# Kernel optimization log

Measured on AMD Instinct MI355X. Metric: run time of the kernel, lower is better.

## Reference

```python
import jax, jax.numpy as jnp
import numpy as np

E = 384      # n_embed
H = 6        # n_head
HS = E // H  # head_size = 64
B = 64
T = 256      # == block_size
FF = 4 * E


def _layernorm(x, g, b, eps=1e-5):
    m = x.mean(-1, keepdims=True)
    v = ((x - m) ** 2).mean(-1, keepdims=True)
    return (x - m) / jnp.sqrt(v + eps) * g + b


def _mha(q_in, k_in, v_in, wq, bq, wk, bk, wv, bv, pw, pb):
    # Faithful to source: scale uses q_in's last dim (n_embed=384), NOT head_size,
    # and the causal tril mask is applied even in cross-attention.
    scale = q_in.shape[-1] ** -0.5
    q = jnp.einsum('bte,hes->bhts', q_in, wq) + bq[None, :, None, :]  # [B,H,T1,HS]
    k = jnp.einsum('bue,hes->bhus', k_in, wk) + bk[None, :, None, :]  # [B,H,T2,HS]
    v = jnp.einsum('bue,hes->bhus', v_in, wv) + bv[None, :, None, :]
    wei = jnp.einsum('bhts,bhus->bhtu', q, k) * scale                 # [B,H,T1,T2]
    T1, T2 = q_in.shape[1], k_in.shape[1]
    mask = jnp.tril(jnp.ones((T1, T2), dtype=bool))
    wei = jnp.where(mask[None, None], wei, -jnp.inf)
    wei = jax.nn.softmax(wei, axis=-1)
    out = jnp.einsum('bhtu,bhus->bths', wei, v)                       # [B,T1,H,HS]
    out = out.reshape(out.shape[0], out.shape[1], -1)                 # concat heads
    return out @ pw + pb


def setup_inputs() -> dict:
    key = jax.random.key(0)
    ks = jax.random.split(key, 32)
    s = 0.02
    d = {
        'encode_output': jax.random.normal(ks[0], (B, T, E), jnp.float32),
        'x': jax.random.normal(ks[1], (B, T, E), jnp.float32),
    }
    i = 2
    for p in ('sa1', 'sa2'):
        d[p + '_wq'] = jax.random.normal(ks[i], (H, E, HS), jnp.float32) * s; i += 1
        d[p + '_bq'] = jnp.zeros((H, HS), jnp.float32)
        d[p + '_wk'] = jax.random.normal(ks[i], (H, E, HS), jnp.float32) * s; i += 1
        d[p + '_bk'] = jnp.zeros((H, HS), jnp.float32)
        d[p + '_wv'] = jax.random.normal(ks[i], (H, E, HS), jnp.float32) * s; i += 1
        d[p + '_bv'] = jnp.zeros((H, HS), jnp.float32)
        d[p + '_pw'] = jax.random.normal(ks[i], (E, E), jnp.float32) * s; i += 1
        d[p + '_pb'] = jnp.zeros((E,), jnp.float32)
    d['ff_w1'] = jax.random.normal(ks[i], (E, FF), jnp.float32) * s; i += 1
    d['ff_b1'] = jnp.zeros((FF,), jnp.float32)
    d['ff_w2'] = jax.random.normal(ks[i], (FF, E), jnp.float32) * s; i += 1
    d['ff_b2'] = jnp.zeros((E,), jnp.float32)
    for n in ('ln1', 'ln2', 'ln3'):
        d[n + '_g'] = jnp.ones((E,), jnp.float32)
        d[n + '_b'] = jnp.zeros((E,), jnp.float32)
    return d


def reference(encode_output, x,
              sa1_wq, sa1_bq, sa1_wk, sa1_bk, sa1_wv, sa1_bv, sa1_pw, sa1_pb,
              sa2_wq, sa2_bq, sa2_wk, sa2_bk, sa2_wv, sa2_bv, sa2_pw, sa2_pb,
              ff_w1, ff_b1, ff_w2, ff_b2,
              ln1_g, ln1_b, ln2_g, ln2_b, ln3_g, ln3_b):
    # masked self-attention + add&norm
    a1 = _mha(x, x, x, sa1_wq, sa1_bq, sa1_wk, sa1_bk, sa1_wv, sa1_bv, sa1_pw, sa1_pb)
    o1 = _layernorm(x + a1, ln1_g, ln1_b)
    # cross-attention (q=o1, k=v=encode_output) + add&norm
    a2 = _mha(o1, encode_output, encode_output,
              sa2_wq, sa2_bq, sa2_wk, sa2_bk, sa2_wv, sa2_bv, sa2_pw, sa2_pb)
    o2 = _layernorm(o1 + a2, ln2_g, ln2_b)
    # FFN + add&norm
    f = jax.nn.relu(o2 @ ff_w1 + ff_b1) @ ff_w2 + ff_b2
    return _layernorm(o2 + f, ln3_g, ln3_b)
```

## Files before the change

### kernel.cpp

```cpp
#include <hip/hip_runtime.h>

typedef __attribute__((ext_vector_type(8))) short bf16x8;
typedef __attribute__((ext_vector_type(4))) float f32x4;

__device__ __forceinline__ float b2f(ushort b) {
    union { unsigned int u; float f; } x;
    x.u = ((unsigned int)b) << 16;
    return x.f;
}
__device__ __forceinline__ ushort f2b(float f) {
    union { float f; unsigned int u; } x;
    x.f = f;
    unsigned int r = x.u + 0x7fffu + ((x.u >> 16) & 1u);
    return (ushort)(r >> 16);
}
__device__ __forceinline__ int4 pack8(float4 a, float4 b) {
    union { int4 v; ushort u[8]; } r;
    r.u[0] = f2b(a.x); r.u[1] = f2b(a.y); r.u[2] = f2b(a.z); r.u[3] = f2b(a.w);
    r.u[4] = f2b(b.x); r.u[5] = f2b(b.y); r.u[6] = f2b(b.z); r.u[7] = f2b(b.w);
    return r.v;
}

__global__ __launch_bounds__(256) void gemm_bt(
    const ushort* __restrict__ A, const ushort* __restrict__ Bt,
    ushort* __restrict__ C, const float* __restrict__ bias,
    const ushort* __restrict__ resb, const float* __restrict__ resf,
    int M, int N, int K, int relu)
{
    __shared__ __align__(16) ushort As[128 * 32];
    __shared__ __align__(16) ushort Bs[128 * 32];
    const int tid  = threadIdx.x;
    const int wave = tid >> 6, lane = tid & 63;
    const int wm = wave >> 1, wn = wave & 1;
    const int qd = lane >> 4, lc = lane & 15;
    const int row0 = blockIdx.y * 128, col0 = blockIdx.x * 128;

    const int srow = tid >> 1;
    const int scol = (tid & 1) * 16;
    const ushort* Ag = A  + (size_t)(row0 + srow) * K + scol;
    const ushort* Bg = Bt + (size_t)(col0 + srow) * K + scol;
    ushort* Asd = &As[srow * 32 + scol];
    ushort* Bsd = &Bs[srow * 32 + scol];

    f32x4 acc[4][4];
#pragma unroll
    for (int i = 0; i < 4; i++)
#pragma unroll
        for (int j = 0; j < 4; j++) acc[i][j] = 0.0f;

    int4 a0 = *(const int4*)(Ag);
    int4 a1 = *(const int4*)(Ag + 8);
    int4 b0 = *(const int4*)(Bg);
    int4 b1 = *(const int4*)(Bg + 8);

    for (int k0 = 0; k0 < K; k0 += 32) {
        __syncthreads();
        *(int4*)Asd = a0; *(int4*)(Asd + 8) = a1;
        *(int4*)Bsd = b0; *(int4*)(Bsd + 8) = b1;
        if (k0 + 32 < K) {
            a0 = *(const int4*)(Ag + k0 + 32);
            a1 = *(const int4*)(Ag + k0 + 40);
            b0 = *(const int4*)(Bg + k0 + 32);
            b1 = *(const int4*)(Bg + k0 + 40);
        }
        __syncthreads();

        bf16x8 af[4], bfr[4];
#pragma unroll
        for (int mi = 0; mi < 4; mi++)
            af[mi] = *(const bf16x8*)&As[(wm * 64 + mi * 16 + lc) * 32 + qd * 8];
#pragma unroll
        for (int ni = 0; ni < 4; ni++)
            bfr[ni] = *(const bf16x8*)&Bs[(wn * 64 + ni * 16 + lc) * 32 + qd * 8];
#pragma unroll
        for (int mi = 0; mi < 4; mi++)
#pragma unroll
            for (int ni = 0; ni < 4; ni++)
                acc[mi][ni] = __builtin_amdgcn_mfma_f32_16x16x32_bf16(
                    af[mi], bfr[ni], acc[mi][ni], 0, 0, 0);
    }

#pragma unroll
    for (int mi = 0; mi < 4; mi++) {
#pragma unroll
        for (int r = 0; r < 4; r++) {
            int grow = row0 + wm * 64 + mi * 16 + qd * 4 + r;
#pragma unroll
            for (int ni = 0; ni < 4; ni++) {
                int gcol = col0 + wn * 64 + ni * 16 + lc;
                float v = acc[mi][ni][r];
                if (bias) v += bias[gcol];
                if (resb) v += b2f(resb[(size_t)grow * N + gcol]);
                if (resf) v += resf[(size_t)grow * N + gcol];
                if (relu) v = fmaxf(v, 0.0f);
                C[(size_t)grow * N + gcol] = f2b(v);
            }
        }
    }
}

__global__ __launch_bounds__(256) void gemm_n64(
    const ushort* __restrict__ A, const ushort* __restrict__ Bt,
    ushort* __restrict__ C, const float* __restrict__ bias,
    const ushort* __restrict__ resb, const float* __restrict__ resf,
    int M, int N, int K, int relu)
{
    __shared__ __align__(16) ushort As[128 * 32];
    __shared__ __align__(16) ushort Bs[64 * 32];
    const int tid  = threadIdx.x;
    const int wave = tid >> 6, lane = tid & 63;
    const int qd = lane >> 4, lc = lane & 15;
    const int row0 = blockIdx.y * 128, col0 = blockIdx.x * 64;

    const int srow = tid >> 1;
    const int scol = (tid & 1) * 16;
    const ushort* Ag = A + (size_t)(row0 + srow) * K + scol;
    ushort* Asd = &As[srow * 32 + scol];
    const int brow = tid >> 2;
    const int bcol = (tid & 3) * 8;
    const ushort* Bg = Bt + (size_t)(col0 + brow) * K + bcol;
    ushort* Bsd = &Bs[brow * 32 + bcol];

    f32x4 acc[2][4];
#pragma unroll
    for (int i = 0; i < 2; i++)
#pragma unroll
        for (int j = 0; j < 4; j++) acc[i][j] = 0.0f;

    int4 a0 = *(const int4*)(Ag);
    int4 a1 = *(const int4*)(Ag + 8);
    int4 b0 = *(const int4*)(Bg);

    for (int k0 = 0; k0 < K; k0 += 32) {
        __syncthreads();
        *(int4*)Asd = a0; *(int4*)(Asd + 8) = a1;
        *(int4*)Bsd = b0;
        if (k0 + 32 < K) {
            a0 = *(const int4*)(Ag + k0 + 32);
            a1 = *(const int4*)(Ag + k0 + 40);
            b0 = *(const int4*)(Bg + k0 + 32);
        }
        __syncthreads();

        bf16x8 af[2], bfr[4];
#pragma unroll
        for (int mi = 0; mi < 2; mi++)
            af[mi] = *(const bf16x8*)&As[(wave * 32 + mi * 16 + lc) * 32 + qd * 8];
#pragma unroll
        for (int ni = 0; ni < 4; ni++)
            bfr[ni] = *(const bf16x8*)&Bs[(ni * 16 + lc) * 32 + qd * 8];
#pragma unroll
        for (int mi = 0; mi < 2; mi++)
#pragma unroll
            for (int ni = 0; ni < 4; ni++)
                acc[mi][ni] = __builtin_amdgcn_mfma_f32_16x16x32_bf16(
                    af[mi], bfr[ni], acc[mi][ni], 0, 0, 0);
    }

#pragma unroll
    for (int mi = 0; mi < 2; mi++) {
#pragma unroll
        for (int r = 0; r < 4; r++) {
            int grow = row0 + wave * 32 + mi * 16 + qd * 4 + r;
#pragma unroll
            for (int ni = 0; ni < 4; ni++) {
                int gcol = col0 + ni * 16 + lc;
                float v = acc[mi][ni][r];
                if (bias) v += bias[gcol];
                if (resb) v += b2f(resb[(size_t)grow * N + gcol]);
                if (resf) v += resf[(size_t)grow * N + gcol];
                if (relu) v = fmaxf(v, 0.0f);
                C[(size_t)grow * N + gcol] = f2b(v);
            }
        }
    }
}

__global__ __launch_bounds__(256) void gemm_dual(
    const ushort* __restrict__ A1, const ushort* __restrict__ B1t,
    ushort* __restrict__ C1, const float* __restrict__ bias1, int N1,
    const ushort* __restrict__ A2, const ushort* __restrict__ B2t,
    ushort* __restrict__ C2, const float* __restrict__ bias2, int N2,
    int split, int K)
{
    __shared__ __align__(16) ushort As[128 * 32];
    __shared__ __align__(16) ushort Bs[64 * 32];
    const int tid  = threadIdx.x;
    const int wave = tid >> 6, lane = tid & 63;
    const int qd = lane >> 4, lc = lane & 15;
    const bool first = (int)blockIdx.x < split;
    const ushort* A  = first ? A1 : A2;
    const ushort* Bt = first ? B1t : B2t;
    ushort* C        = first ? C1 : C2;
    const float* bias = first ? bias1 : bias2;
    const int N      = first ? N1 : N2;
    const int col0   = (first ? blockIdx.x : blockIdx.x - split) * 64;
    const int row0   = blockIdx.y * 128;

    const int srow = tid >> 1;
    const int scol = (tid & 1) * 16;
    const ushort* Ag = A + (size_t)(row0 + srow) * K + scol;
    ushort* Asd = &As[srow * 32 + scol];
    const int brow = tid >> 2;
    const int bcol = (tid & 3) * 8;
    const ushort* Bg = Bt + (size_t)(col0 + brow) * K + bcol;
    ushort* Bsd = &Bs[brow * 32 + bcol];

    f32x4 acc[2][4];
#pragma unroll
    for (int i = 0; i < 2; i++)
#pragma unroll
        for (int j = 0; j < 4; j++) acc[i][j] = 0.0f;

    int4 a0 = *(const int4*)(Ag);
    int4 a1 = *(const int4*)(Ag + 8);
    int4 b0 = *(const int4*)(Bg);

    for (int k0 = 0; k0 < K; k0 += 32) {
        __syncthreads();
        *(int4*)Asd = a0; *(int4*)(Asd + 8) = a1;
        *(int4*)Bsd = b0;
        if (k0 + 32 < K) {
            a0 = *(const int4*)(Ag + k0 + 32);
            a1 = *(const int4*)(Ag + k0 + 40);
            b0 = *(const int4*)(Bg + k0 + 32);
        }
        __syncthreads();

        bf16x8 af[2], bfr[4];
#pragma unroll
        for (int mi = 0; mi < 2; mi++)
            af[mi] = *(const bf16x8*)&As[(wave * 32 + mi * 16 + lc) * 32 + qd * 8];
#pragma unroll
        for (int ni = 0; ni < 4; ni++)
            bfr[ni] = *(const bf16x8*)&Bs[(ni * 16 + lc) * 32 + qd * 8];
#pragma unroll
        for (int mi = 0; mi < 2; mi++)
#pragma unroll
            for (int ni = 0; ni < 4; ni++)
                acc[mi][ni] = __builtin_amdgcn_mfma_f32_16x16x32_bf16(
                    af[mi], bfr[ni], acc[mi][ni], 0, 0, 0);
    }

#pragma unroll
    for (int mi = 0; mi < 2; mi++) {
#pragma unroll
        for (int r = 0; r < 4; r++) {
            int grow = row0 + wave * 32 + mi * 16 + qd * 4 + r;
#pragma unroll
            for (int ni = 0; ni < 4; ni++) {
                int gcol = col0 + ni * 16 + lc;
                float v = acc[mi][ni][r] + bias[gcol];
                C[(size_t)grow * N + gcol] = f2b(v);
            }
        }
    }
}

__global__ __launch_bounds__(256) void attn(
    const ushort* __restrict__ q, int qstr,
    const ushort* __restrict__ k, int kstr,
    const ushort* __restrict__ v, int vstr,
    ushort* __restrict__ out)
{
    __shared__ __align__(16) ushort Qs[64 * 72];
    __shared__ __align__(16) ushort Kc[64 * 72];
    __shared__ __align__(16) ushort Vc[64 * 72];
    __shared__ __align__(16) ushort Ps[64 * 264];

    const int tid = threadIdx.x;
    const int wave = tid >> 6, lane = tid & 63;
    const int qd = lane >> 4, lc = lane & 15;
    const int b = blockIdx.z, h = blockIdx.y, t0 = blockIdx.x * 64;
    const int hc = h * 64;
    const float scale = 0.051031036307982884f;

    {
        int r = tid >> 2, c = (tid & 3) * 16;
        int4 q0 = *(const int4*)&q[(size_t)(b * 256 + t0 + r) * qstr + hc + c];
        int4 q1 = *(const int4*)&q[(size_t)(b * 256 + t0 + r) * qstr + hc + c + 8];
        *(int4*)&Qs[r * 72 + c] = q0;
        *(int4*)&Qs[r * 72 + c + 8] = q1;
    }

    f32x4 accS[16];
#pragma unroll
    for (int j = 0; j < 16; j++) accS[j] = 0.0f;

    for (int uc = 0; uc < 4; uc++) {
        int r = tid >> 2, c = (tid & 3) * 16;
        int4 k0v = *(const int4*)&k[(size_t)(b * 256 + uc * 64 + r) * kstr + hc + c];
        int4 k1v = *(const int4*)&k[(size_t)(b * 256 + uc * 64 + r) * kstr + hc + c + 8];
        __syncthreads();
        *(int4*)&Kc[r * 72 + c] = k0v;
        *(int4*)&Kc[r * 72 + c + 8] = k1v;
        __syncthreads();
#pragma unroll
        for (int s0 = 0; s0 < 64; s0 += 32) {
            bf16x8 a = *(const bf16x8*)&Qs[(wave * 16 + lc) * 72 + s0 + qd * 8];
#pragma unroll
            for (int ni = 0; ni < 4; ni++) {
                bf16x8 bb = *(const bf16x8*)&Kc[(ni * 16 + lc) * 72 + s0 + qd * 8];
                accS[uc * 4 + ni] =
                    __builtin_amdgcn_mfma_f32_16x16x32_bf16(a, bb, accS[uc * 4 + ni], 0, 0, 0);
            }
        }
    }

#pragma unroll
    for (int rr = 0; rr < 4; rr++) {
        int t = t0 + wave * 16 + qd * 4 + rr;
        float pv[16];
        float mx = -3.0e38f;
#pragma unroll
        for (int j = 0; j < 16; j++) {
            int u = (j >> 2) * 64 + (j & 3) * 16 + lc;
            float s = accS[j][rr] * scale;
            s = (u <= t) ? s : -3.0e38f;
            pv[j] = s;
            mx = fmaxf(mx, s);
        }
#pragma unroll
        for (int m = 1; m < 16; m <<= 1) mx = fmaxf(mx, __shfl_xor(mx, m, 16));
        float sum = 0.0f;
#pragma unroll
        for (int j = 0; j < 16; j++) { float p = __expf(pv[j] - mx); pv[j] = p; sum += p; }
#pragma unroll
        for (int m = 1; m < 16; m <<= 1) sum += __shfl_xor(sum, m, 16);
        float inv = 1.0f / sum;
#pragma unroll
        for (int j = 0; j < 16; j++) {
            int u = (j >> 2) * 64 + (j & 3) * 16 + lc;
            Ps[(wave * 16 + qd * 4 + rr) * 264 + u] = f2b(pv[j] * inv);
        }
    }

    f32x4 accO[4];
#pragma unroll
    for (int j = 0; j < 4; j++) accO[j] = 0.0f;
    for (int uc = 0; uc < 4; uc++) {
        int r = tid >> 2, s0 = (tid & 3) * 16;
        int4 v0 = *(const int4*)&v[(size_t)(b * 256 + uc * 64 + r) * vstr + hc + s0];
        int4 v1 = *(const int4*)&v[(size_t)(b * 256 + uc * 64 + r) * vstr + hc + s0 + 8];
        __syncthreads();
        {
            const ushort* t0p = (const ushort*)&v0;
            const ushort* t1p = (const ushort*)&v1;
#pragma unroll
            for (int j = 0; j < 8; j++) Vc[(s0 + j) * 72 + r] = t0p[j];
#pragma unroll
            for (int j = 0; j < 8; j++) Vc[(s0 + 8 + j) * 72 + r] = t1p[j];
        }
        __syncthreads();
#pragma unroll
        for (int u0 = 0; u0 < 64; u0 += 32) {
            bf16x8 a = *(const bf16x8*)&Ps[(wave * 16 + lc) * 264 + uc * 64 + u0 + qd * 8];
#pragma unroll
            for (int ni = 0; ni < 4; ni++) {
                bf16x8 bb = *(const bf16x8*)&Vc[(ni * 16 + lc) * 72 + u0 + qd * 8];
                accO[ni] = __builtin_amdgcn_mfma_f32_16x16x32_bf16(a, bb, accO[ni], 0, 0, 0);
            }
        }
    }

#pragma unroll
    for (int ni = 0; ni < 4; ni++)
#pragma unroll
        for (int rr = 0; rr < 4; rr++) {
            int t = t0 + wave * 16 + qd * 4 + rr;
            out[(size_t)(b * 256 + t) * 384 + hc + ni * 16 + lc] = f2b(accO[ni][rr]);
        }
}

__global__ __launch_bounds__(256) void lnorm(
    const ushort* __restrict__ in, const float* __restrict__ g,
    const float* __restrict__ be, ushort* __restrict__ outb,
    float* __restrict__ outf)
{
    const int wave = threadIdx.x >> 6, lane = threadIdx.x & 63;
    const int row = blockIdx.x * 4 + wave;
    const ushort* r = in + (size_t)row * 384;
    float x[6], s1 = 0.0f, s2 = 0.0f;
#pragma unroll
    for (int j = 0; j < 6; j++) {
        x[j] = b2f(r[j * 64 + lane]);
        s1 += x[j]; s2 += x[j] * x[j];
    }
#pragma unroll
    for (int m = 1; m < 64; m <<= 1) {
        s1 += __shfl_xor(s1, m, 64);
        s2 += __shfl_xor(s2, m, 64);
    }
    float mean = s1 * (1.0f / 384.0f);
    float var  = s2 * (1.0f / 384.0f) - mean * mean;
    float rstd = rsqrtf(var + 1e-5f);
#pragma unroll
    for (int j = 0; j < 6; j++) {
        float y = (x[j] - mean) * rstd * g[j * 64 + lane] + be[j * 64 + lane];
        if (outb) outb[(size_t)row * 384 + j * 64 + lane] = f2b(y);
        if (outf) outf[(size_t)row * 384 + j * 64 + lane] = y;
    }
}

__device__ __forceinline__ void dev_cvt(const float* in, ushort* out, int blk) {
    size_t i = ((size_t)blk * 256 + threadIdx.x) * 8;
    float4 a = *(const float4*)(in + i);
    float4 b = *(const float4*)(in + i + 4);
    *(int4*)(out + i) = pack8(a, b);
}
__device__ __forceinline__ void dev_transp(const float* in, ushort* out,
                                           int R, int C, int bx, int by,
                                           float (*t)[33]) {
    const int tx = threadIdx.x & 31, ty = threadIdx.x >> 5;
    const int c0 = bx * 32, r0 = by * 32;
#pragma unroll
    for (int i = 0; i < 32; i += 8)
        t[ty + i][tx] = in[(size_t)(r0 + ty + i) * C + c0 + tx];
    __syncthreads();
#pragma unroll
    for (int i = 0; i < 32; i += 8)
        out[(size_t)(c0 + ty + i) * R + r0 + tx] = f2b(t[tx][ty + i]);
}
__device__ __forceinline__ void dev_packqkv(const float* wq, const float* wk,
                                            const float* wv, ushort* Wt,
                                            int blk, float (*t)[33]) {
    const int tx = threadIdx.x & 31, ty = threadIdx.x >> 5;
    const int bx = blk % 12, by = (blk / 12) % 2, bz = blk / 24;
    const int e0 = bx * 32, s0 = by * 32;
    const int seg = bz / 6, h = bz - seg * 6;
    const float* w = (seg == 0) ? wq : (seg == 1) ? wk : wv;
    const float* wh = w + (size_t)h * 384 * 64;
#pragma unroll
    for (int i = 0; i < 32; i += 8)
        t[ty + i][tx] = wh[(size_t)(e0 + ty + i) * 64 + s0 + tx];
    __syncthreads();
    const int nbase = seg * 384 + h * 64 + s0;
#pragma unroll
    for (int i = 0; i < 32; i += 8)
        Wt[(size_t)(nbase + ty + i) * 384 + e0 + tx] = f2b(t[tx][ty + i]);
}

__global__ __launch_bounds__(256) void prep_all(
    const float* __restrict__ x, ushort* __restrict__ xb,
    const float* __restrict__ enc, ushort* __restrict__ encb,
    const float* __restrict__ s1wq, const float* __restrict__ s1wk,
    const float* __restrict__ s1wv, ushort* __restrict__ W1,
    const float* __restrict__ s2wq, const float* __restrict__ s2wk,
    const float* __restrict__ s2wv, ushort* __restrict__ W2,
    const float* __restrict__ s1pw, ushort* __restrict__ pw1t,
    const float* __restrict__ s2pw, ushort* __restrict__ pw2t,
    const float* __restrict__ fw1, ushort* __restrict__ w1t,
    const float* __restrict__ fw2, ushort* __restrict__ w2t,
    const float* __restrict__ s1bq, const float* __restrict__ s1bk,
    const float* __restrict__ s1bv, const float* __restrict__ s2bq,
    const float* __restrict__ s2bk, const float* __restrict__ s2bv,
    float* __restrict__ bias1, float* __restrict__ bias2)
{
    __shared__ float t[32][33];
    int blk = blockIdx.x;
    if (blk < 3072) { dev_cvt(x, xb, blk); return; }
    blk -= 3072;
    if (blk < 3072) { dev_cvt(enc, encb, blk); return; }
    blk -= 3072;
    if (blk < 432) { dev_packqkv(s1wq, s1wk, s1wv, W1, blk, t); return; }
    blk -= 432;
    if (blk < 432) { dev_packqkv(s2wq, s2wk, s2wv, W2, blk, t); return; }
    blk -= 432;
    if (blk < 144) { dev_transp(s1pw, pw1t, 384, 384, blk % 12, blk / 12, t); return; }
    blk -= 144;
    if (blk < 144) { dev_transp(s2pw, pw2t, 384, 384, blk % 12, blk / 12, t); return; }
    blk -= 144;
    if (blk < 576) { dev_transp(fw1, w1t, 384, 1536, blk % 48, blk / 48, t); return; }
    blk -= 576;
    if (blk < 576) { dev_transp(fw2, w2t, 1536, 384, blk % 12, blk / 12, t); return; }
    blk -= 576;
    int i = blk * 256 + threadIdx.x;
    if (i >= 2304) return;
    int grp = i / 1152, r = i - grp * 1152;
    int seg = r / 384, nn = r - seg * 384;
    const float* src = grp == 0 ? (seg == 0 ? s1bq : seg == 1 ? s1bk : s1bv)
                                : (seg == 0 ? s2bq : seg == 1 ? s2bk : s2bv);
    (grp == 0 ? bias1 : bias2)[r] = src[nn];
}

extern "C" void kernel_launch(void* const* d_in, const int* in_sizes, int n_in,
                              void* d_out, int out_size, void* d_ws, size_t ws_size,
                              hipStream_t stream)
{
    const float* enc = (const float*)d_in[0];
    const float* x   = (const float*)d_in[1];
    const float* s1wq = (const float*)d_in[2];  const float* s1bq = (const float*)d_in[3];
    const float* s1wk = (const float*)d_in[4];  const float* s1bk = (const float*)d_in[5];
    const float* s1wv = (const float*)d_in[6];  const float* s1bv = (const float*)d_in[7];
    const float* s1pw = (const float*)d_in[8];  const float* s1pb = (const float*)d_in[9];
    const float* s2wq = (const float*)d_in[10]; const float* s2bq = (const float*)d_in[11];
    const float* s2wk = (const float*)d_in[12]; const float* s2bk = (const float*)d_in[13];
    const float* s2wv = (const float*)d_in[14]; const float* s2bv = (const float*)d_in[15];
    const float* s2pw = (const float*)d_in[16]; const float* s2pb = (const float*)d_in[17];
    const float* fw1 = (const float*)d_in[18];  const float* fb1 = (const float*)d_in[19];
    const float* fw2 = (const float*)d_in[20];  const float* fb2 = (const float*)d_in[21];
    const float* g1 = (const float*)d_in[22];   const float* be1 = (const float*)d_in[23];
    const float* g2 = (const float*)d_in[24];   const float* be2 = (const float*)d_in[25];
    const float* g3 = (const float*)d_in[26];   const float* be3 = (const float*)d_in[27];

    if (ws_size < 80216064u) return;

    ushort* wsp = (ushort*)d_ws;
    ushort* qkv1 = wsp;
    ushort* q2   = wsp;
    ushort* kv2  = wsp + 6291456;
    ushort* h1   = wsp;
    ushort* att  = wsp + 18874368;
    ushort* xb   = wsp + 18874368;
    ushort* tmp  = wsp + 25165824;
    ushort* o1b  = wsp + 31457280;
    ushort* W1   = wsp + 37748736;
    ushort* W2   = W1 + 442368;
    ushort* pw1t = W2 + 442368;
    ushort* pw2t = pw1t + 147456;
    ushort* w1t  = pw2t + 147456;
    ushort* w2t  = w1t + 589824;

    ushort* encb = (ushort*)d_out;
    ushort* o2b  = (ushort*)d_out;
    float* bias1 = (float*)((ushort*)d_out + 6291456);
    float* bias2 = bias1 + 1152;

    prep_all<<<dim3(8457), dim3(256), 0, stream>>>(
        x, xb, enc, encb,
        s1wq, s1wk, s1wv, W1, s2wq, s2wk, s2wv, W2,
        s1pw, pw1t, s2pw, pw2t, fw1, w1t, fw2, w2t,
        s1bq, s1bk, s1bv, s2bq, s2bk, s2bv, bias1, bias2);

    gemm_bt<<<dim3(9, 128), dim3(256), 0, stream>>>(xb, W1, qkv1, bias1, nullptr, nullptr, 16384, 1152, 384, 0);
    attn<<<dim3(4, 6, 64), dim3(256), 0, stream>>>(qkv1, 1152, qkv1 + 384, 1152, qkv1 + 768, 1152, att);
    gemm_n64<<<dim3(6, 128), dim3(256), 0, stream>>>(att, pw1t, tmp, s1pb, nullptr, x, 16384, 384, 384, 0);
    lnorm<<<dim3(4096), dim3(256), 0, stream>>>(tmp, g1, be1, o1b, nullptr);

    gemm_dual<<<dim3(18, 128), dim3(256), 0, stream>>>(
        o1b, W2, q2, bias2, 384,
        encb, W2 + 147456, kv2, bias2 + 384, 768, 6, 384);
    attn<<<dim3(4, 6, 64), dim3(256), 0, stream>>>(q2, 384, kv2, 768, kv2 + 384, 768, att);
    gemm_n64<<<dim3(6, 128), dim3(256), 0, stream>>>(att, pw2t, tmp, s2pb, o1b, nullptr, 16384, 384, 384, 0);
    lnorm<<<dim3(4096), dim3(256), 0, stream>>>(tmp, g2, be2, o2b, nullptr);

    gemm_bt<<<dim3(12, 128), dim3(256), 0, stream>>>(o2b, w1t, h1, fb1, nullptr, nullptr, 16384, 1536, 384, 1);
    gemm_n64<<<dim3(6, 128), dim3(256), 0, stream>>>(h1, w2t, tmp, fb2, o2b, nullptr, 16384, 384, 1536, 0);
    lnorm<<<dim3(4096), dim3(256), 0, stream>>>(tmp, g3, be3, nullptr, (float*)d_out);
}
```

Before: 498.7 us.

## Stage GEMM epilogues through LDS for vectorized stores and remap blocks per XCD

Result: faster. 457.1 us (-8.3%).

```diff
diff --git a/kernel.cpp b/kernel.cpp
--- a/kernel.cpp
+++ b/kernel.cpp
@@ -20,20 +20,40 @@
     r.u[4] = f2b(b.x); r.u[5] = f2b(b.y); r.u[6] = f2b(b.z); r.u[7] = f2b(b.w);
     return r.v;
 }
+__device__ __forceinline__ int4 add_resb(int4 cs, int4 rs) {
+    const ushort* c = (const ushort*)&cs; const ushort* r = (const ushort*)&rs;
+    union { int4 v; ushort u[8]; } o;
+#pragma unroll
+    for (int j = 0; j < 8; j++) o.u[j] = f2b(b2f(c[j]) + b2f(r[j]));
+    return o.v;
+}
+__device__ __forceinline__ int4 add_resf(int4 cs, float4 r0, float4 r1) {
+    const ushort* c = (const ushort*)&cs;
+    const float* rf0 = (const float*)&r0; const float* rf1 = (const float*)&r1;
+    union { int4 v; ushort u[8]; } o;
+#pragma unroll
+    for (int j = 0; j < 4; j++) o.u[j] = f2b(b2f(c[j]) + rf0[j]);
+#pragma unroll
+    for (int j = 0; j < 4; j++) o.u[4 + j] = f2b(b2f(c[4 + j]) + rf1[j]);
+    return o.v;
+}
 
 __global__ __launch_bounds__(256) void gemm_bt(
     const ushort* __restrict__ A, const ushort* __restrict__ Bt,
     ushort* __restrict__ C, const float* __restrict__ bias,
     const ushort* __restrict__ resb, const float* __restrict__ resf,
-    int M, int N, int K, int relu)
+    int N, int K, int relu)
 {
     __shared__ __align__(16) ushort As[128 * 32];
     __shared__ __align__(16) ushort Bs[128 * 32];
+    __shared__ __align__(16) ushort Cs[64 * 132];
     const int tid  = threadIdx.x;
     const int wave = tid >> 6, lane = tid & 63;
     const int wm = wave >> 1, wn = wave & 1;
     const int qd = lane >> 4, lc = lane & 15;
-    const int row0 = blockIdx.y * 128, col0 = blockIdx.x * 128;
+    const int id = blockIdx.x, xcd = id & 7, sub = id >> 3;
+    const int row0 = (xcd * 16 + (sub & 15)) * 128;
+    const int col0 = (sub >> 4) * 128;
 
     const int srow = tid >> 1;
     const int scol = (tid & 1) * 16;
@@ -81,20 +101,33 @@
     }
 
 #pragma unroll
-    for (int mi = 0; mi < 4; mi++) {
-#pragma unroll
-        for (int r = 0; r < 4; r++) {
-            int grow = row0 + wm * 64 + mi * 16 + qd * 4 + r;
-#pragma unroll
-            for (int ni = 0; ni < 4; ni++) {
-                int gcol = col0 + wn * 64 + ni * 16 + lc;
-                float v = acc[mi][ni][r];
-                if (bias) v += bias[gcol];
-                if (resb) v += b2f(resb[(size_t)grow * N + gcol]);
-                if (resf) v += resf[(size_t)grow * N + gcol];
-                if (relu) v = fmaxf(v, 0.0f);
-                C[(size_t)grow * N + gcol] = f2b(v);
-            }
+    for (int half = 0; half < 2; half++) {
+        __syncthreads();
+        if (wm == half) {
+#pragma unroll
+            for (int mi = 0; mi < 4; mi++)
+#pragma unroll
+                for (int r = 0; r < 4; r++) {
+                    int lr = mi * 16 + qd * 4 + r;
+#pragma unroll
+                    for (int ni = 0; ni < 4; ni++) {
+                        float v = acc[mi][ni][r];
+                        if (bias) v += bias[col0 + wn * 64 + ni * 16 + lc];
+                        if (relu) v = fmaxf(v, 0.0f);
+                        Cs[lr * 132 + wn * 64 + ni * 16 + lc] = f2b(v);
+                    }
+                }
+        }
+        __syncthreads();
+        int lr = tid >> 2, cc = (tid & 3) * 32;
+        size_t base = (size_t)(row0 + half * 64 + lr) * N + col0 + cc;
+#pragma unroll
+        for (int i = 0; i < 4; i++) {
+            int4 d = *(const int4*)&Cs[lr * 132 + cc + i * 8];
+            if (resb) d = add_resb(d, *(const int4*)&resb[base + i * 8]);
+            else if (resf) d = add_resf(d, *(const float4*)&resf[base + i * 8],
+                                           *(const float4*)&resf[base + i * 8 + 4]);
+            *(int4*)&C[base + i * 8] = d;
         }
     }
 }
@@ -103,14 +136,17 @@
     const ushort* __restrict__ A, const ushort* __restrict__ Bt,
     ushort* __restrict__ C, const float* __restrict__ bias,
     const ushort* __restrict__ resb, const float* __restrict__ resf,
-    int M, int N, int K, int relu)
+    int N, int K, int relu)
 {
     __shared__ __align__(16) ushort As[128 * 32];
     __shared__ __align__(16) ushort Bs[64 * 32];
+    __shared__ __align__(16) ushort Cs[128 * 68];
     const int tid  = threadIdx.x;
     const int wave = tid >> 6, lane = tid & 63;
     const int qd = lane >> 4, lc = lane & 15;
-    const int row0 = blockIdx.y * 128, col0 = blockIdx.x * 64;
+    const int id = blockIdx.x, xcd = id & 7, sub = id >> 3;
+    const int row0 = (xcd * 16 + (sub & 15)) * 128;
+    const int col0 = (sub >> 4) * 64;
 
     const int srow = tid >> 1;
     const int scol = (tid & 1) * 16;
@@ -157,21 +193,31 @@
                     af[mi], bfr[ni], acc[mi][ni], 0, 0, 0);
     }
 
-#pragma unroll
-    for (int mi = 0; mi < 2; mi++) {
+    __syncthreads();
+#pragma unroll
+    for (int mi = 0; mi < 2; mi++)
 #pragma unroll
         for (int r = 0; r < 4; r++) {
-            int grow = row0 + wave * 32 + mi * 16 + qd * 4 + r;
+            int lr = wave * 32 + mi * 16 + qd * 4 + r;
 #pragma unroll
             for (int ni = 0; ni < 4; ni++) {
-                int gcol = col0 + ni * 16 + lc;
                 float v = acc[mi][ni][r];
-                if (bias) v += bias[gcol];
-                if (resb) v += b2f(resb[(size_t)grow * N + gcol]);
-                if (resf) v += resf[(size_t)grow * N + gcol];
+                if (bias) v += bias[col0 + ni * 16 + lc];
                 if (relu) v = fmaxf(v, 0.0f);
-                C[(size_t)grow * N + gcol] = f2b(v);
+                Cs[lr * 68 + ni * 16 + lc] = f2b(v);
             }
+        }
+    __syncthreads();
+    {
+        int lr = tid >> 1, cc = (tid & 1) * 32;
+        size_t base = (size_t)(row0 + lr) * N + col0 + cc;
+#pragma unroll
+        for (int i = 0; i < 4; i++) {
+            int4 d = *(const int4*)&Cs[lr * 68 + cc + i * 8];
+            if (resb) d = add_resb(d, *(const int4*)&resb[base + i * 8]);
+            else if (resf) d = add_resf(d, *(const float4*)&resf[base + i * 8],
+                                           *(const float4*)&resf[base + i * 8 + 4]);
+            *(int4*)&C[base + i * 8] = d;
         }
     }
 }
@@ -185,17 +231,20 @@
 {
     __shared__ __align__(16) ushort As[128 * 32];
     __shared__ __align__(16) ushort Bs[64 * 32];
+    __shared__ __align__(16) ushort Cs[128 * 68];
     const int tid  = threadIdx.x;
     const int wave = tid >> 6, lane = tid & 63;
     const int qd = lane >> 4, lc = lane & 15;
-    const bool first = (int)blockIdx.x < split;
+    const int id = blockIdx.x, xcd = id & 7, sub = id >> 3;
+    const int row0 = (xcd * 16 + (sub & 15)) * 128;
+    int ct = sub >> 4;
+    const bool first = ct < split;
     const ushort* A  = first ? A1 : A2;
     const ushort* Bt = first ? B1t : B2t;
     ushort* C        = first ? C1 : C2;
     const float* bias = first ? bias1 : bias2;
     const int N      = first ? N1 : N2;
-    const int col0   = (first ? blockIdx.x : blockIdx.x - split) * 64;
-    const int row0   = blockIdx.y * 128;
+    const int col0   = (first ? ct : ct - split) * 64;
 
     const int srow = tid >> 1;
     const int scol = (tid & 1) * 16;
@@ -242,18 +291,23 @@
                     af[mi], bfr[ni], acc[mi][ni], 0, 0, 0);
     }
 
-#pragma unroll
-    for (int mi = 0; mi < 2; mi++) {
+    __syncthreads();
+#pragma unroll
+    for (int mi = 0; mi < 2; mi++)
 #pragma unroll
         for (int r = 0; r < 4; r++) {
-            int grow = row0 + wave * 32 + mi * 16 + qd * 4 + r;
-#pragma unroll
-            for (int ni = 0; ni < 4; ni++) {
-                int gcol = col0 + ni * 16 + lc;
-                float v = acc[mi][ni][r] + bias[gcol];
-                C[(size_t)grow * N + gcol] = f2b(v);
-            }
-        }
+            int lr = wave * 32 + mi * 16 + qd * 4 + r;
+#pragma unroll
+            for (int ni = 0; ni < 4; ni++)
+                Cs[lr * 68 + ni * 16 + lc] = f2b(acc[mi][ni][r] + bias[col0 + ni * 16 + lc]);
+        }
+    __syncthreads();
+    {
+        int lr = tid >> 1, cc = (tid & 1) * 32;
+        size_t base = (size_t)(row0 + lr) * N + col0 + cc;
+#pragma unroll
+        for (int i = 0; i < 4; i++)
+            *(int4*)&C[base + i * 8] = *(const int4*)&Cs[lr * 68 + cc + i * 8];
     }
 }
 
@@ -532,19 +586,19 @@
         s1pw, pw1t, s2pw, pw2t, fw1, w1t, fw2, w2t,
         s1bq, s1bk, s1bv, s2bq, s2bk, s2bv, bias1, bias2);
 
-    gemm_bt<<<dim3(9, 128), dim3(256), 0, stream>>>(xb, W1, qkv1, bias1, nullptr, nullptr, 16384, 1152, 384, 0);
+    gemm_bt<<<dim3(9 * 128), dim3(256), 0, stream>>>(xb, W1, qkv1, bias1, nullptr, nullptr, 1152, 384, 0);
     attn<<<dim3(4, 6, 64), dim3(256), 0, stream>>>(qkv1, 1152, qkv1 + 384, 1152, qkv1 + 768, 1152, att);
-    gemm_n64<<<dim3(6, 128), dim3(256), 0, stream>>>(att, pw1t, tmp, s1pb, nullptr, x, 16384, 384, 384, 0);
+    gemm_n64<<<dim3(6 * 128), dim3(256), 0, stream>>>(att, pw1t, tmp, s1pb, nullptr, x, 384, 384, 0);
     lnorm<<<dim3(4096), dim3(256), 0, stream>>>(tmp, g1, be1, o1b, nullptr);
 
-    gemm_dual<<<dim3(18, 128), dim3(256), 0, stream>>>(
+    gemm_dual<<<dim3(18 * 128), dim3(256), 0, stream>>>(
         o1b, W2, q2, bias2, 384,
         encb, W2 + 147456, kv2, bias2 + 384, 768, 6, 384);
     attn<<<dim3(4, 6, 64), dim3(256), 0, stream>>>(q2, 384, kv2, 768, kv2 + 384, 768, att);
-    gemm_n64<<<dim3(6, 128), dim3(256), 0, stream>>>(att, pw2t, tmp, s2pb, o1b, nullptr, 16384, 384, 384, 0);
+    gemm_n64<<<dim3(6 * 128), dim3(256), 0, stream>>>(att, pw2t, tmp, s2pb, o1b, nullptr, 384, 384, 0);
     lnorm<<<dim3(4096), dim3(256), 0, stream>>>(tmp, g2, be2, o2b, nullptr);
 
-    gemm_bt<<<dim3(12, 128), dim3(256), 0, stream>>>(o2b, w1t, h1, fb1, nullptr, nullptr, 16384, 1536, 384, 1);
-    gemm_n64<<<dim3(6, 128), dim3(256), 0, stream>>>(h1, w2t, tmp, fb2, o2b, nullptr, 16384, 384, 1536, 0);
+    gemm_bt<<<dim3(12 * 128), dim3(256), 0, stream>>>(o2b, w1t, h1, fb1, nullptr, nullptr, 1536, 384, 1);
+    gemm_n64<<<dim3(6 * 128), dim3(256), 0, stream>>>(h1, w2t, tmp, fb2, o2b, nullptr, 384, 1536, 0);
     lnorm<<<dim3(4096), dim3(256), 0, stream>>>(tmp, g3, be3, nullptr, (float*)d_out);
 }
```
